# Optimization experiments

Hardware: AMD Instinct MI355X
Metric: run time of the kernel (lower is better)

The kernel has to match this reference:

```python
import jax, jax.numpy as jnp
import numpy as np

N = 100000
H = 8      # heads
C = 8      # out channels per head
NEG_SLOPE = 0.2
EPS = 1e-16


def setup_inputs() -> dict:
    key = jax.random.key(0)
    k1, k2, k3, k4, k5, k6 = jax.random.split(key, 6)
    x = jax.random.normal(k1, (N, 128), dtype=jnp.float32)
    edge_index = jax.random.randint(k2, (2, 1600000), 0, N, dtype=jnp.int64)
    W = jax.random.normal(k3, (128, H * C), dtype=jnp.float32) * (1.0 / np.sqrt(128))
    att_src = jax.random.normal(k4, (H, C), dtype=jnp.float32)
    att_dst = jax.random.normal(k5, (H, C), dtype=jnp.float32)
    bias = jax.random.normal(k6, (H * C,), dtype=jnp.float32) * 0.01
    return {"x": x, "edge_index": edge_index, "W": W,
            "att_src": att_src, "att_dst": att_dst, "bias": bias}


def _gat_forward(x, edge_index, W, att_src, att_dst, bias):
    # add self loops (PyG GATConv default add_self_loops=True)
    loop = jnp.arange(N, dtype=edge_index.dtype)
    src = jnp.concatenate([edge_index[0], loop])
    dst = jnp.concatenate([edge_index[1], loop])

    h = (x @ W).reshape(N, H, C)                       # [N,H,C]
    a_src = jnp.sum(h * att_src, axis=-1)              # [N,H]
    a_dst = jnp.sum(h * att_dst, axis=-1)              # [N,H]

    e = a_src[src] + a_dst[dst]                        # [E,H]
    e = jnp.where(e > 0, e, NEG_SLOPE * e)             # leaky_relu(0.2)

    # segment softmax over edges grouped by destination node
    m = jax.ops.segment_max(e, dst, num_segments=N)    # [N,H]
    m = jnp.where(jnp.isfinite(m), m, 0.0)
    ex = jnp.exp(e - m[dst])                           # [E,H]
    denom = jax.ops.segment_sum(ex, dst, num_segments=N)
    alpha = ex / (denom[dst] + EPS)                    # [E,H]

    msg = alpha[:, :, None] * h[src]                   # [E,H,C]
    out = jax.ops.segment_sum(msg, dst, num_segments=N)  # [N,H,C]
    out = out.reshape(N, H * C) + bias
    return jax.nn.relu(out)


def reference(x, edge_index, W, att_src, att_dst, bias):
    return _gat_forward(x, edge_index, W, att_src, att_dst, bias)
```

## Files before the change

kernel.cpp:

```cpp
#include <hip/hip_runtime.h>
#include <hip/hip_bf16.h>

#define NNODES 100000
#define NH 8
#define OUTD 64
#define FDIM 128
#define NEG_SLOPE 0.2f
#define NBUCK ((NNODES + 255) / 256)
#define MAXB 5376
#define CH 8192
#define ROWS_PB 128
#define NFB ((NNODES + ROWS_PB - 1) / ROWS_PB)
#define SHST 68

typedef __attribute__((ext_vector_type(8))) short bf16x8;
typedef __attribute__((ext_vector_type(4))) float f32x4;

static __device__ __forceinline__ unsigned short f2bf(float f) {
    __hip_bfloat16 b = __float2bfloat16(f);
    return *(unsigned short*)&b;
}

__global__ __launch_bounds__(256) void k_featbin(
    const float* __restrict__ x, const float* __restrict__ W,
    const float* __restrict__ att_s, const float* __restrict__ att_d,
    const int* __restrict__ ei, int E,
    __hip_bfloat16* __restrict__ h, float* __restrict__ asrc,
    float* __restrict__ adst, int* __restrict__ gCur,
    unsigned int* __restrict__ gSorted)
{
    int tid = threadIdx.x;

    if (blockIdx.x >= NFB) {
        __shared__ int cnt[NBUCK];
        __shared__ int base[NBUCK];
        int tot = E + NNODES;
        int e0 = (blockIdx.x - NFB) * CH;
        int e1 = e0 + CH; if (e1 > tot) e1 = tot;

        for (int i = tid; i < NBUCK; i += 256) cnt[i] = 0;
        __syncthreads();

        for (int i = e0 + tid; i < e1; i += 256) {
            int d = (i < E) ? ei[E + i] : (i - E);
            atomicAdd(&cnt[d >> 8], 1);
        }
        __syncthreads();

        for (int i = tid; i < NBUCK; i += 256) {
            int c = cnt[i];
            base[i] = (c > 0) ? atomicAdd(&gCur[i], c) : 0;
            cnt[i] = 0;
        }
        __syncthreads();

        for (int i = e0 + tid; i < e1; i += 256) {
            int s, d;
            if (i < E) { s = ei[i]; d = ei[E + i]; }
            else       { s = d = i - E; }
            int b = d >> 8;
            int p = base[b] + atomicAdd(&cnt[b], 1);
            if (p < MAXB)
                gSorted[(size_t)b * MAXB + p] =
                    ((unsigned int)(d & 255) << 17) | (unsigned int)s;
        }
        return;
    }

    __shared__ unsigned short sx[ROWS_PB * FDIM];
    __shared__ unsigned short swt[OUTD * FDIM];
    __shared__ float shf[4 * 16 * SHST];
    __shared__ float sAs[OUTD], sAd[OUTD];

    if (tid < OUTD) { sAs[tid] = att_s[tid]; sAd[tid] = att_d[tid]; }

    for (int i = tid; i < OUTD * 16; i += 256) {
        int col = i & 63, chunk = i >> 6;
        unsigned short tmp[8];
#pragma unroll
        for (int j = 0; j < 8; ++j)
            tmp[j] = f2bf(W[(chunk * 8 + j) * OUTD + col]);
        int chs = chunk ^ (col & 15);
        *(bf16x8*)&swt[col * FDIM + chs * 8] = *(bf16x8*)tmp;
    }
    int row0 = blockIdx.x * ROWS_PB;
    for (int c = tid; c < ROWS_PB * 16; c += 256) {
        int row = c >> 4, chunk = c & 15;
        int grow = row0 + row;
        unsigned short tmp[8];
        if (grow < NNODES) {
            const float* p = x + (size_t)grow * FDIM + chunk * 8;
            f32x4 f0 = *(const f32x4*)p;
            f32x4 f1 = *(const f32x4*)(p + 4);
#pragma unroll
            for (int j = 0; j < 4; ++j) tmp[j] = f2bf(f0[j]);
#pragma unroll
            for (int j = 0; j < 4; ++j) tmp[4 + j] = f2bf(f1[j]);
        } else {
#pragma unroll
            for (int j = 0; j < 8; ++j) tmp[j] = 0;
        }
        int chs = chunk ^ (row & 15);
        *(bf16x8*)&sx[row * FDIM + chs * 8] = *(bf16x8*)tmp;
    }
    __syncthreads();

    int w = tid >> 6, l = tid & 63;
    int l4 = l & 15, g = l >> 4;

    bf16x8 bfrag[16];
#pragma unroll
    for (int n = 0; n < 4; ++n)
#pragma unroll
        for (int kk = 0; kk < 4; ++kk) {
            int col = n * 16 + l4;
            int chs = (kk * 4 + g) ^ l4;
            bfrag[n * 4 + kk] = *(const bf16x8*)&swt[col * FDIM + chs * 8];
        }

    float* mysh = &shf[w * 16 * SHST];

#pragma unroll
    for (int rt = 0; rt < 2; ++rt) {
        int lbase = w * 32 + rt * 16;
        f32x4 acc[4];
#pragma unroll
        for (int n = 0; n < 4; ++n) acc[n] = (f32x4){0.f, 0.f, 0.f, 0.f};

#pragma unroll
        for (int kk = 0; kk < 4; ++kk) {
            int row = lbase + l4;
            int chs = (kk * 4 + g) ^ l4;
            bf16x8 a = *(const bf16x8*)&sx[row * FDIM + chs * 8];
#pragma unroll
            for (int n = 0; n < 4; ++n)
                acc[n] = __builtin_amdgcn_mfma_f32_16x16x32_bf16(
                    a, bfrag[n * 4 + kk], acc[n], 0, 0, 0);
        }

#pragma unroll
        for (int n = 0; n < 4; ++n)
#pragma unroll
            for (int r = 0; r < 4; ++r)
                mysh[(g * 4 + r) * SHST + n * 16 + l4] = acc[n][r];

#pragma unroll
        for (int i = 0; i < 2; ++i) {
            int c = i * 64 + l;
            int row = c >> 3, ch = c & 7;
            int grow = row0 + lbase + row;
            if (grow < NNODES) {
                const float* rp = &mysh[row * SHST + ch * 8];
                unsigned short tmp[8];
#pragma unroll
                for (int j = 0; j < 8; ++j) tmp[j] = f2bf(rp[j]);
                *(bf16x8*)&h[(size_t)grow * OUTD + ch * 8] = *(bf16x8*)tmp;
            }
        }
#pragma unroll
        for (int i = 0; i < 2; ++i) {
            int t = i * 64 + l;
            int row = t >> 3, hd = t & 7;
            int grow = row0 + lbase + row;
            if (grow < NNODES) {
                const float* rp = &mysh[row * SHST + hd * 8];
                float s1 = 0.f, s2 = 0.f;
#pragma unroll
                for (int j = 0; j < 8; ++j) {
                    s1 = fmaf(rp[j], sAs[hd * 8 + j], s1);
                    s2 = fmaf(rp[j], sAd[hd * 8 + j], s2);
                }
                asrc[grow * NH + hd] = s1;
                adst[grow * NH + hd] = s2;
            }
        }
    }
}

__global__ __launch_bounds__(256) void k_csr(
    const int* __restrict__ gCur, unsigned int* __restrict__ gSorted,
    int2* __restrict__ rows)
{
    __shared__ unsigned int ent[MAXB];
    __shared__ int cnt[256], cur[256];
    __shared__ int wsum[4];
    int b = blockIdx.x;
    int n = gCur[b]; if (n > MAXB) n = MAXB;
    size_t gbase = (size_t)b * MAXB;
    int tid = threadIdx.x;

    for (int i = tid; i < n; i += 256) ent[i] = gSorted[gbase + i];
    cnt[tid] = 0;
    __syncthreads();

    for (int i = tid; i < n; i += 256)
        atomicAdd(&cnt[ent[i] >> 17], 1);
    __syncthreads();

    int v = cnt[tid];
    int lane = tid & 63, wid = tid >> 6;
    int acc = v;
#pragma unroll
    for (int off = 1; off < 64; off <<= 1) {
        int t = __shfl_up(acc, off);
        if (lane >= off) acc += t;
    }
    if (lane == 63) wsum[wid] = acc;
    __syncthreads();
    int woff = 0;
#pragma unroll
    for (int i = 0; i < 4; ++i) woff += (i < wid) ? wsum[i] : 0;
    int ex = acc + woff - v;

    int node = (b << 8) + tid;
    if (node < NNODES)
        rows[node] = make_int2((int)gbase + ex, (int)gbase + ex + v);
    cur[tid] = ex;
    __syncthreads();

    for (int i = tid; i < n; i += 256) {
        unsigned int p = ent[i];
        int pos = atomicAdd(&cur[p >> 17], 1);
        gSorted[gbase + pos] = p & 0x1FFFFu;
    }
}

__global__ __launch_bounds__(256) void k_gather(
    const int2* __restrict__ rows, const unsigned int* __restrict__ esrc,
    const __hip_bfloat16* __restrict__ h, const float* __restrict__ asrc,
    const float* __restrict__ adst, const float* __restrict__ bias,
    float* __restrict__ out)
{
    int node = (blockIdx.x * 256 + threadIdx.x) >> 6;
    if (node >= NNODES) return;
    int lane = threadIdx.x & 63;
    int slot = lane >> 4;
    int li   = lane & 15;
    int hh   = li >> 1;

    float adh = adst[(unsigned)(node * NH + hh)];
    int2 se = rows[node];
    const uint2* hu = (const uint2*)h;

    float n0 = 0.f, n1 = 0.f, n2 = 0.f, n3 = 0.f, den = 0.f;

    for (int base = se.x; base < se.y; base += 64) {
        int cnt = se.y - base; if (cnt > 64) cnt = 64;
        int sj = (lane < cnt) ? (int)esrc[base + lane] : 0;

        int k = 0;
        for (; k + 8 <= cnt; k += 8) {
            int sA = __shfl(sj, k + slot);
            int sB = __shfl(sj, k + 4 + slot);
            float aA = asrc[(unsigned)(sA * NH + hh)];
            float aB = asrc[(unsigned)(sB * NH + hh)];
            uint2 wA = hu[(unsigned)(sA * 16 + li)];
            uint2 wB = hu[(unsigned)(sB * 16 + li)];
            float eA = aA + adh; eA = fmaxf(eA, NEG_SLOPE * eA); eA = __expf(eA);
            float eB = aB + adh; eB = fmaxf(eB, NEG_SLOPE * eB); eB = __expf(eB);
            den += eA; den += eB;
            union { unsigned u; float f; } t;
            t.u = wA.x << 16;         n0 = fmaf(eA, t.f, n0);
            t.u = wA.x & 0xffff0000u; n1 = fmaf(eA, t.f, n1);
            t.u = wA.y << 16;         n2 = fmaf(eA, t.f, n2);
            t.u = wA.y & 0xffff0000u; n3 = fmaf(eA, t.f, n3);
            t.u = wB.x << 16;         n0 = fmaf(eB, t.f, n0);
            t.u = wB.x & 0xffff0000u; n1 = fmaf(eB, t.f, n1);
            t.u = wB.y << 16;         n2 = fmaf(eB, t.f, n2);
            t.u = wB.y & 0xffff0000u; n3 = fmaf(eB, t.f, n3);
        }
        for (; k < cnt; k += 4) {
            int s2 = __shfl(sj, k + slot);
            bool valid = (k + slot) < cnt;
            float a = asrc[(unsigned)(s2 * NH + hh)];
            uint2 w = hu[(unsigned)(s2 * 16 + li)];
            float e = a + adh; e = fmaxf(e, NEG_SLOPE * e);
            float ex = valid ? __expf(e) : 0.f;
            den += ex;
            union { unsigned u; float f; } t;
            t.u = w.x << 16;         n0 = fmaf(ex, t.f, n0);
            t.u = w.x & 0xffff0000u; n1 = fmaf(ex, t.f, n1);
            t.u = w.y << 16;         n2 = fmaf(ex, t.f, n2);
            t.u = w.y & 0xffff0000u; n3 = fmaf(ex, t.f, n3);
        }
    }

    n0 += __shfl_xor(n0, 16); n0 += __shfl_xor(n0, 32);
    n1 += __shfl_xor(n1, 16); n1 += __shfl_xor(n1, 32);
    n2 += __shfl_xor(n2, 16); n2 += __shfl_xor(n2, 32);
    n3 += __shfl_xor(n3, 16); n3 += __shfl_xor(n3, 32);
    den += __shfl_xor(den, 16); den += __shfl_xor(den, 32);

    if (slot == 0) {
        float inv = 1.f / (den + 1e-16f);
        int ch = li * 4;
        float4 v;
        v.x = fmaxf(n0 * inv + bias[ch + 0], 0.f);
        v.y = fmaxf(n1 * inv + bias[ch + 1], 0.f);
        v.z = fmaxf(n2 * inv + bias[ch + 2], 0.f);
        v.w = fmaxf(n3 * inv + bias[ch + 3], 0.f);
        *(float4*)&out[(unsigned)(node * OUTD + ch)] = v;
    }
}

extern "C" void kernel_launch(void* const* d_in, const int* in_sizes, int n_in,
                              void* d_out, int out_size, void* d_ws, size_t ws_size,
                              hipStream_t stream)
{
    const float* x     = (const float*)d_in[0];
    const int*   ei    = (const int*)  d_in[1];
    const float* W     = (const float*)d_in[2];
    const float* att_s = (const float*)d_in[3];
    const float* att_d = (const float*)d_in[4];
    const float* bias  = (const float*)d_in[5];
    float* out = (float*)d_out;
    int E = in_sizes[1] / 2;
    int tot = E + NNODES;

    __hip_bfloat16* h = (__hip_bfloat16*)d_ws;
    float* asrc   = (float*)(h + (size_t)NNODES * OUTD);
    float* adst   = asrc + (size_t)NNODES * NH;
    int2*  rows   = (int2*)(adst + (size_t)NNODES * NH);
    int*   gCur   = (int*)(rows + NNODES);
    unsigned int* gSorted = (unsigned int*)(gCur + 512);

    hipMemsetAsync(gCur, 0, 512 * sizeof(int), stream);

    int nbin = (tot + CH - 1) / CH;
    k_featbin<<<NFB + nbin, 256, 0, stream>>>(x, W, att_s, att_d, ei, E,
                                              h, asrc, adst, gCur, gSorted);
    k_csr<<<NBUCK, 256, 0, stream>>>(gCur, gSorted, rows);
    k_gather<<<(NNODES * 64 + 255) / 256, 256, 0, stream>>>(
        rows, gSorted, h, asrc, adst, bias, out);
}
```

Baseline: 116.5 us.

## Load x directly into MFMA registers and compute attention logits via shuffles

The feature-transform path no longer stages the 128x128 bf16 x tile in shared memory. Each lane loads its own x row slice straight from global into registers, converts it to bf16, and feeds it to the MFMA. Attention logits are now computed from the accumulators with cross-lane xor shuffles rather than re-reading an fp32 staging buffer. The staging buffer for h is also shrunk to bf16. This cuts LDS use and barriers, which could raise occupancy, at the cost of less coalesced global loads of x and more shuffle instructions.

```diff
diff --git a/kernel.cpp b/kernel.cpp
--- a/kernel.cpp
+++ b/kernel.cpp
@@ -11,7 +11,7 @@
 #define CH 8192
 #define ROWS_PB 128
 #define NFB ((NNODES + ROWS_PB - 1) / ROWS_PB)
-#define SHST 68
+#define HSTRIDE 68
 
 typedef __attribute__((ext_vector_type(8))) short bf16x8;
 typedef __attribute__((ext_vector_type(4))) float f32x4;
@@ -67,12 +67,10 @@
         return;
     }
 
-    __shared__ unsigned short sx[ROWS_PB * FDIM];
     __shared__ unsigned short swt[OUTD * FDIM];
-    __shared__ float shf[4 * 16 * SHST];
-    __shared__ float sAs[OUTD], sAd[OUTD];
-
-    if (tid < OUTD) { sAs[tid] = att_s[tid]; sAd[tid] = att_d[tid]; }
+    __shared__ unsigned short shb[4 * 16 * HSTRIDE];
+    __shared__ float slgs[4 * 128];
+    __shared__ float slgd[4 * 128];
 
     for (int i = tid; i < OUTD * 16; i += 256) {
         int col = i & 63, chunk = i >> 6;
@@ -83,30 +81,11 @@
         int chs = chunk ^ (col & 15);
         *(bf16x8*)&swt[col * FDIM + chs * 8] = *(bf16x8*)tmp;
     }
-    int row0 = blockIdx.x * ROWS_PB;
-    for (int c = tid; c < ROWS_PB * 16; c += 256) {
-        int row = c >> 4, chunk = c & 15;
-        int grow = row0 + row;
-        unsigned short tmp[8];
-        if (grow < NNODES) {
-            const float* p = x + (size_t)grow * FDIM + chunk * 8;
-            f32x4 f0 = *(const f32x4*)p;
-            f32x4 f1 = *(const f32x4*)(p + 4);
-#pragma unroll
-            for (int j = 0; j < 4; ++j) tmp[j] = f2bf(f0[j]);
-#pragma unroll
-            for (int j = 0; j < 4; ++j) tmp[4 + j] = f2bf(f1[j]);
-        } else {
-#pragma unroll
-            for (int j = 0; j < 8; ++j) tmp[j] = 0;
-        }
-        int chs = chunk ^ (row & 15);
-        *(bf16x8*)&sx[row * FDIM + chs * 8] = *(bf16x8*)tmp;
-    }
     __syncthreads();
 
     int w = tid >> 6, l = tid & 63;
     int l4 = l & 15, g = l >> 4;
+    int row0 = blockIdx.x * ROWS_PB;
 
     bf16x8 bfrag[16];
 #pragma unroll
@@ -118,31 +97,74 @@
             bfrag[n * 4 + kk] = *(const bf16x8*)&swt[col * FDIM + chs * 8];
         }
 
-    float* mysh = &shf[w * 16 * SHST];
+    float as_r[4], ad_r[4];
+#pragma unroll
+    for (int n = 0; n < 4; ++n) {
+        as_r[n] = att_s[n * 16 + l4];
+        ad_r[n] = att_d[n * 16 + l4];
+    }
+
+    unsigned short* myh = &shb[w * 16 * HSTRIDE];
+    float* myls = &slgs[w * 128];
+    float* myld = &slgd[w * 128];
 
 #pragma unroll
     for (int rt = 0; rt < 2; ++rt) {
         int lbase = w * 32 + rt * 16;
+        int grow_a = row0 + lbase + l4;
+        bool va = grow_a < NNODES;
+
+        f32x4 xa[8];
+        const float* xp = x + (size_t)grow_a * FDIM + g * 8;
+        if (va) {
+#pragma unroll
+            for (int kk = 0; kk < 4; ++kk) {
+                xa[2 * kk]     = *(const f32x4*)(xp + kk * 32);
+                xa[2 * kk + 1] = *(const f32x4*)(xp + kk * 32 + 4);
+            }
+        } else {
+#pragma unroll
+            for (int i = 0; i < 8; ++i) xa[i] = (f32x4){0.f, 0.f, 0.f, 0.f};
+        }
+        bf16x8 af[4];
+#pragma unroll
+        for (int kk = 0; kk < 4; ++kk)
+#pragma unroll
+            for (int j = 0; j < 4; ++j) {
+                af[kk][j]     = (short)f2bf(xa[2 * kk][j]);
+                af[kk][4 + j] = (short)f2bf(xa[2 * kk + 1][j]);
+            }
+
         f32x4 acc[4];
 #pragma unroll
         for (int n = 0; n < 4; ++n) acc[n] = (f32x4){0.f, 0.f, 0.f, 0.f};
-
-#pragma unroll
-        for (int kk = 0; kk < 4; ++kk) {
-            int row = lbase + l4;
-            int chs = (kk * 4 + g) ^ l4;
-            bf16x8 a = *(const bf16x8*)&sx[row * FDIM + chs * 8];
+#pragma unroll
+        for (int kk = 0; kk < 4; ++kk)
 #pragma unroll
             for (int n = 0; n < 4; ++n)
                 acc[n] = __builtin_amdgcn_mfma_f32_16x16x32_bf16(
-                    a, bfrag[n * 4 + kk], acc[n], 0, 0, 0);
-        }
+                    af[kk], bfrag[n * 4 + kk], acc[n], 0, 0, 0);
 
 #pragma unroll
         for (int n = 0; n < 4; ++n)
 #pragma unroll
             for (int r = 0; r < 4; ++r)
-                mysh[(g * 4 + r) * SHST + n * 16 + l4] = acc[n][r];
+                myh[(g * 4 + r) * HSTRIDE + n * 16 + l4] = f2bf(acc[n][r]);
+
+#pragma unroll
+        for (int n = 0; n < 4; ++n)
+#pragma unroll
+            for (int r = 0; r < 4; ++r) {
+                float vs = acc[n][r] * as_r[n];
+                float vd = acc[n][r] * ad_r[n];
+                vs += __shfl_xor(vs, 1); vs += __shfl_xor(vs, 2); vs += __shfl_xor(vs, 4);
+                vd += __shfl_xor(vd, 1); vd += __shfl_xor(vd, 2); vd += __shfl_xor(vd, 4);
+                if ((l & 7) == 0) {
+                    int row = g * 4 + r, hd = 2 * n + (l4 >> 3);
+                    myls[row * 8 + hd] = vs;
+                    myld[row * 8 + hd] = vd;
+                }
+            }
 
 #pragma unroll
         for (int i = 0; i < 2; ++i) {
@@ -150,28 +172,18 @@
             int row = c >> 3, ch = c & 7;
             int grow = row0 + lbase + row;
             if (grow < NNODES) {
-                const float* rp = &mysh[row * SHST + ch * 8];
-                unsigned short tmp[8];
-#pragma unroll
-                for (int j = 0; j < 8; ++j) tmp[j] = f2bf(rp[j]);
-                *(bf16x8*)&h[(size_t)grow * OUTD + ch * 8] = *(bf16x8*)tmp;
+                bf16x8 v = *(const bf16x8*)&myh[row * HSTRIDE + ch * 8];
+                *(bf16x8*)&h[(size_t)grow * OUTD + ch * 8] = v;
             }
         }
 #pragma unroll
         for (int i = 0; i < 2; ++i) {
-            int t = i * 64 + l;
-            int row = t >> 3, hd = t & 7;
+            int c = i * 64 + l;
+            int row = c >> 3, hd = c & 7;
             int grow = row0 + lbase + row;
             if (grow < NNODES) {
-                const float* rp = &mysh[row * SHST + hd * 8];
-                float s1 = 0.f, s2 = 0.f;
-#pragma unroll
-                for (int j = 0; j < 8; ++j) {
-                    s1 = fmaf(rp[j], sAs[hd * 8 + j], s1);
-                    s2 = fmaf(rp[j], sAd[hd * 8 + j], s2);
-                }
-                asrc[grow * NH + hd] = s1;
-                adst[grow * NH + hd] = s2;
+                asrc[grow * NH + hd] = myls[row * 8 + hd];
+                adst[grow * NH + hd] = myld[row * 8 + hd];
             }
         }
     }
```

Result: no change. 115.0 us (-1.3%).
